# Performance work log

Measured on AMD Instinct MI355X. Metric: run time of the kernel, lower is better.

The kernel has to match this reference:

```python
import jax, jax.numpy as jnp
import numpy as np

B, F, T, Z, Y, X = 1, 8, 5, 16, 96, 96
N_RAYS = 32768   # n_rays_scan
K = 128          # n_points_ray
NEAR_PLANE = 0.01
C = F * Z        # conv channels after folding Z into channel dim


def setup_inputs() -> dict:
    key = jax.random.key(0)
    ks = jax.random.split(key, 6)
    vol = jax.random.normal(ks[0], (B, F, T, Z, Y, X), jnp.float32)
    # ray origins inside the normalized unit-cube scene
    rays_o = jax.random.uniform(ks[1], (T, N_RAYS, 3), jnp.float32, 0.1, 0.9)
    rd = jax.random.normal(ks[2], (T, N_RAYS, 3), jnp.float32)
    rays_d = rd / jnp.linalg.norm(rd, axis=-1, keepdims=True)
    conv_w = jax.random.normal(ks[3], (C, C, 3, 3, 3), jnp.float32) * (1.0 / np.sqrt(C * 27))
    conv_b = jnp.zeros((C,), jnp.float32)
    dens_w = jax.random.normal(ks[4], (F, 1), jnp.float32) * (1.0 / np.sqrt(F))
    dens_b = jnp.zeros((1,), jnp.float32)
    return dict(curr_feat_volume=vol, ray_start=rays_o, ray_direction=rays_d,
                conv_w=conv_w, conv_b=conv_b, dens_w=dens_w, dens_b=dens_b)


def _trilinear(vol, pts):
    """vol: [F,Z,Y,X]; pts: [...,3] with (x,y,z) in [0,1]. Returns [..., F]."""
    Fc, Zs, Ys, Xs = vol.shape
    gx = jnp.clip(pts[..., 0], 0.0, 1.0) * (Xs - 1)
    gy = jnp.clip(pts[..., 1], 0.0, 1.0) * (Ys - 1)
    gz = jnp.clip(pts[..., 2], 0.0, 1.0) * (Zs - 1)
    x0 = jnp.floor(gx).astype(jnp.int32); x1 = jnp.minimum(x0 + 1, Xs - 1)
    y0 = jnp.floor(gy).astype(jnp.int32); y1 = jnp.minimum(y0 + 1, Ys - 1)
    z0 = jnp.floor(gz).astype(jnp.int32); z1 = jnp.minimum(z0 + 1, Zs - 1)
    fx = gx - x0; fy = gy - y0; fz = gz - z0
    out = 0.0
    for zi, wz in ((z0, 1 - fz), (z1, fz)):
        for yi, wy in ((y0, 1 - fy), (y1, fy)):
            for xi, wx in ((x0, 1 - fx), (x1, fx)):
                out = out + vol[:, zi, yi, xi] * (wz * wy * wx)[None]
    return jnp.moveaxis(out, 0, -1)


def _render_t(vol_t, o, d, dens_w, dens_b):
    """One timestep: vol_t [F,Z,Y,X], o/d [N,3] -> depth [N,1]."""
    # SceneCollider: AABB [0,1]^3 with near_plane clamp
    t1 = (0.0 - o) / d
    t2 = (1.0 - o) / d
    near = jnp.max(jnp.minimum(t1, t2), axis=-1, keepdims=True)
    far = jnp.min(jnp.maximum(t1, t2), axis=-1, keepdims=True)
    near = jnp.maximum(near, NEAR_PLANE)
    far = jnp.maximum(far, near + 1e-6)
    # UniformSampler (deterministic bins)
    bins = jnp.linspace(0.0, 1.0, K + 1, dtype=jnp.float32)
    ts = near + bins[None, :] * (far - near)          # [N,K+1]
    starts = ts[:, :-1, None]                          # [N,K,1]
    ends = ts[:, 1:, None]
    mids = 0.5 * (starts + ends)
    pts = o[:, None, :] + d[:, None, :] * mids         # [N,K,3]
    # DensityField: trilinear feature gather + linear + softplus
    feats = _trilinear(vol_t, pts)                     # [N,K,F]
    density = jax.nn.softplus(feats @ dens_w + dens_b) # [N,K,1]
    # weights / transmittance (alpha compositing)
    deltas = ends - starts
    dd = density * deltas
    trans = jnp.exp(-jnp.concatenate([jnp.zeros_like(dd[:, :1]),
                                      jnp.cumsum(dd[:, :-1], axis=1)], axis=1))
    alpha = 1.0 - jnp.exp(-dd)
    weights = alpha * trans                            # [N,K,1]
    # DepthRenderer
    eps = 1e-10
    depth = jnp.sum(weights * starts, axis=-2) / (jnp.sum(weights, axis=-2) + eps)
    depth = jnp.clip(depth, starts.min(), starts.max())
    return depth                                       # [N,1]


def reference(curr_feat_volume, ray_start, ray_direction, conv_w, conv_b, dens_w, dens_b):
    # fold Z into channels and run dense Conv3d over (T,Y,X)
    x = jnp.transpose(curr_feat_volume, (0, 1, 3, 2, 4, 5)).reshape(B, F * Z, T, Y, X)
    y = jax.lax.conv_general_dilated(
        x, conv_w, window_strides=(1, 1, 1), padding='SAME',
        dimension_numbers=('NCDHW', 'OIDHW', 'NCDHW'))
    y = y + conv_b[None, :, None, None, None]
    future = jnp.transpose(y.reshape(B, F, Z, T, Y, X), (0, 3, 1, 2, 4, 5))  # [B,T,F,Z,Y,X]
    vols = future[0]                                   # [T,F,Z,Y,X]
    depth = jax.vmap(lambda v, o, d: _render_t(v, o, d, dens_w, dens_b))(
        vols, ray_start, ray_direction)                # [T,N,1]
    return depth
```

## Files before the change

### kernel.cpp

```cpp
#include <hip/hip_runtime.h>
#include <hip/hip_fp16.h>
#include <cstdint>
#include <cstddef>

#define T_DIM 5
#define F_DIM 8
#define Z_DIM 16
#define Y_DIM 96
#define X_DIM 96
#define NRAYS 32768
#define K_SAMP 128


struct __align__(16) Cell { __half2 h0, h1, h2, h3; };

typedef __attribute__((ext_vector_type(4))) float     f32x4;
typedef __attribute__((ext_vector_type(8))) _Float16  f16x8;

__device__ __forceinline__ float fexp2(float x) { return __builtin_amdgcn_exp2f(x); }
__device__ __forceinline__ float flog2(float x) { return __builtin_amdgcn_logf(x); }

__global__ __launch_bounds__(256) void setup_kernel(
        const float* __restrict__ xin, __half* __restrict__ inp,
        const float* __restrict__ w, const float* __restrict__ cb,
        const float* __restrict__ dw, __half* __restrict__ wB, float* __restrict__ bR,
        const float* __restrict__ ro, const float* __restrict__ rd,
        float* __restrict__ nearA, float* __restrict__ farA) {
    int b = blockIdx.x;
    if (b < 480) {
        __shared__ __half lds[96 * 136];
        int t = b / 96, y = b - (b / 96) * 96;
        for (int i = threadIdx.x; i < 12288; i += 256) {
            int row = i / 96;
            int x   = i - row * 96;
            int f = row >> 4, z = row & 15;
            float v = xin[(((size_t)(f * 5 + t) * 16 + z) * 96 + y) * 96 + x];
            lds[x * 136 + row] = __float2half(v);
        }
        __syncthreads();
        __half* ob = inp + ((size_t)(t * 96 + y) * 96) * 128;
        for (int c = threadIdx.x; c < 1536; c += 256) {
            int x = c >> 4, sub = c & 15;
            uint4 v = *(const uint4*)(lds + x * 136 + sub * 8);
            *(uint4*)(ob + (size_t)x * 128 + sub * 8) = v;
        }
    } else if (b < 696) {
        int i = (b - 480) * 256 + threadIdx.x;
        if (i < 16) {
            float s = 0.f;
            #pragma unroll
            for (int f = 0; f < 8; ++f) s += cb[f * 16 + i] * dw[f];
            bR[i] = s;
        }
        int cs  = i & 31;
        int zo  = (i >> 5) & 15;
        int pt  = i >> 9;
        int p   = pt / 27;
        int tap = pt - p * 27;
        int ci  = p * 32 + cs;
        float s = 0.f;
        #pragma unroll
        for (int f = 0; f < 8; ++f)
            s += w[(size_t)((f * 16 + zo) * 128 + ci) * 27 + tap] * dw[f];
        wB[i] = __float2half(s);
    } else {
        int gid = (b - 696) * 256 + threadIdx.x;
        const float* o = ro + (size_t)gid * 3;
        const float* d = rd + (size_t)gid * 3;
        float ox = o[0], oy = o[1], oz = o[2];
        float dx = d[0], dy = d[1], dz = d[2];
        float t1x = (0.f - ox) / dx, t2x = (1.f - ox) / dx;
        float t1y = (0.f - oy) / dy, t2y = (1.f - oy) / dy;
        float t1z = (0.f - oz) / dz, t2z = (1.f - oz) / dz;
        float nr = fmaxf(fmaxf(fminf(t1x, t2x), fminf(t1y, t2y)), fminf(t1z, t2z));
        float fr = fminf(fminf(fmaxf(t1x, t2x), fmaxf(t1y, t2y)), fmaxf(t1z, t2z));
        nr = fmaxf(nr, 0.01f);
        fr = fmaxf(fr, nr + 1e-6f);
        nearA[gid] = nr;
        farA[gid]  = fr;
    }
}

__global__ __launch_bounds__(128) void conv_mfma_kernel(
        const __half* __restrict__ inp, const __half* __restrict__ wB,
        float* __restrict__ part) {
    int bid = blockIdx.x;
    int wg  = (bid & 7) * 360 + (bid >> 3);
    int p   = wg & 3;
    int wq  = wg >> 2;
    int xs  = wq % 3;
    int rem = wq / 3;
    int yp  = rem % 48;
    int t   = rem / 48;
    int xseg = xs * 32, y0 = yp * 2;

    __shared__ __half lds[12 * 34 * 32];
    const int w    = threadIdx.x >> 6;
    const int lane = threadIdx.x & 63;
    const int l15  = lane & 15;
    const int ksub = lane >> 4;

    const int xl0 = threadIdx.x >> 2, sub0 = threadIdx.x & 3;
    const int xg0 = xseg + xl0 - 1;
    const bool xok0 = (unsigned)xg0 < 96u;
    const int glo0 = xg0 * 128 + sub0 * 8 + (p << 5);
    const int lof0 = xl0 * 32 + ((sub0 ^ ((xl0 >> 1) & 3)) << 3);
    const int q    = threadIdx.x / 12;
    const int rowh = threadIdx.x - q * 12;
    const int xl1  = 32 + (q >> 2), sub1 = q & 3;
    const int xg1  = xseg + xl1 - 1;
    const bool hwr = (q < 8);
    const bool hld = hwr && ((unsigned)xg1 < 96u);
    const int glo1 = xg1 * 128 + sub1 * 8 + (p << 5);
    const int lof1 = xl1 * 32 + ((sub1 ^ ((xl1 >> 1) & 3)) << 3);

    int offA[3];
    #pragma unroll
    for (int kx = 0; kx < 3; ++kx) {
        int X = l15 + kx;
        offA[kx] = X * 32 + ((ksub ^ ((X >> 1) & 3)) << 3);
    }

    uint4 vm[12];
    #pragma unroll
    for (int r = 0; r < 12; ++r) {
        int tt = t + (r >> 2) - 1;
        int yy = y0 + (r & 3) - 1;
        bool rok = ((unsigned)tt < 5u) & ((unsigned)yy < 96u);
        int rbase = (tt * 96 + yy) * 12288;
        uint4 v = {0u, 0u, 0u, 0u};
        if (rok & xok0) v = *(const uint4*)(inp + rbase + glo0);
        vm[r] = v;
    }
    uint4 vh = {0u, 0u, 0u, 0u};
    {
        int tt = t + (rowh >> 2) - 1;
        int yy = y0 + (rowh & 3) - 1;
        bool rok = ((unsigned)tt < 5u) & ((unsigned)yy < 96u);
        int rbase = (tt * 96 + yy) * 12288;
        if (rok & hld) vh = *(const uint4*)(inp + rbase + glo1);
    }
    #pragma unroll
    for (int r = 0; r < 12; ++r)
        *(uint4*)(lds + r * 1088 + lof0) = vm[r];
    if (hwr)
        *(uint4*)(lds + rowh * 1088 + lof1) = vh;
    __syncthreads();

    f32x4 acc0 = {0.f, 0.f, 0.f, 0.f};
    f32x4 acc1 = {0.f, 0.f, 0.f, 0.f};
    const __half* wp_base = wB + (size_t)p * 13824 + l15 * 32 + ksub * 8;
    #pragma unroll
    for (int kt = 0; kt < 3; ++kt) {
        #pragma unroll
        for (int ky = 0; ky < 3; ++ky) {
            const __half* lrow = lds + (kt * 4 + w + ky) * 1088;
            #pragma unroll
            for (int kx = 0; kx < 3; ++kx) {
                int tap = (kt * 3 + ky) * 3 + kx;
                f16x8 aw = *(const f16x8*)(wp_base + tap * 512);
                f16x8 b0 = *(const f16x8*)(lrow + offA[kx]);
                acc0 = __builtin_amdgcn_mfma_f32_16x16x32_f16(aw, b0, acc0, 0, 0, 0);
                f16x8 b1 = *(const f16x8*)(lrow + offA[kx] + 512);
                acc1 = __builtin_amdgcn_mfma_f32_16x16x32_f16(aw, b1, acc1, 0, 0, 0);
            }
        }
    }

    int yw = y0 + w;
    float* po = part + (size_t)p * 737280;
    #pragma unroll
    for (int r = 0; r < 4; ++r) {
        int zo = ksub * 4 + r;
        size_t o = (((size_t)t * 16 + zo) * 96 + yw) * 96 + xseg + l15;
        po[o]      = acc0[r];
        po[o + 16] = acc1[r];
    }
}

__global__ __launch_bounds__(256) void combpack_kernel(
        const float* __restrict__ part, const float* __restrict__ bR,
        Cell* __restrict__ cellp) {
    int b = blockIdx.x;
    int t = b / 192;
    int r = b - t * 192;
    int z = r / 12;
    int y0 = (r - z * 12) * 8;
    int z1 = min(z + 1, 15);

    __shared__ float Lf[18 * 96];
    const float4* pp = (const float4*)part;
    for (int j = threadIdx.x; j < 432; j += 256) {
        int row = j / 24, xq = j - row * 24;
        int plane = row >= 9;
        int zz = plane ? z1 : z;
        int yy = min(y0 + row - (plane ? 9 : 0), 95);
        size_t f4 = ((size_t)(t * 16 + zz) * 96 + yy) * 24 + xq;
        float bz = bR[zz];
        float4 a0 = pp[f4];
        float4 a1 = pp[f4 + 184320];
        float4 a2 = pp[f4 + 2 * 184320];
        float4 a3 = pp[f4 + 3 * 184320];
        float4 s;
        s.x = bz + a0.x + a1.x + a2.x + a3.x;
        s.y = bz + a0.y + a1.y + a2.y + a3.y;
        s.z = bz + a0.z + a1.z + a2.z + a3.z;
        s.w = bz + a0.w + a1.w + a2.w + a3.w;
        *(float4*)(Lf + row * 96 + xq * 4) = s;
    }
    __syncthreads();

    const size_t tz = (size_t)(t * 16 + z);
    #pragma unroll
    for (int k = 0; k < 3; ++k) {
        int c = threadIdx.x + k * 256;
        int yl = c / 96, x = c - yl * 96;
        int xp = min(x + 1, 95);
        float c000 = Lf[yl * 96 + x],        c001 = Lf[yl * 96 + xp];
        float c010 = Lf[(yl + 1) * 96 + x],  c011 = Lf[(yl + 1) * 96 + xp];
        float c100 = Lf[(9 + yl) * 96 + x],  c101 = Lf[(9 + yl) * 96 + xp];
        float c110 = Lf[(10 + yl) * 96 + x], c111 = Lf[(10 + yl) * 96 + xp];
        Cell cl;
        cl.h0 = __floats2half2_rn(c000, c001 - c000);
        cl.h1 = __floats2half2_rn(c010, c011 - c010);
        cl.h2 = __floats2half2_rn(c100, c101 - c100);
        cl.h3 = __floats2half2_rn(c110, c111 - c110);
        cellp[(tz * 96 + y0 + yl) * 96 + x] = cl;
    }
}

__global__ __launch_bounds__(256) void render_kernel(
        const float* __restrict__ ro, const float* __restrict__ rd,
        const Cell* __restrict__ cellp,
        const float* __restrict__ nearA, const float* __restrict__ farA,
        const float* __restrict__ dens_b, float* __restrict__ out) {
    int b = blockIdx.x;
    int b7 = b & 7, bhi = b >> 3;
    int t, seg;
    if (b7 < 5) { t = b7; seg = bhi; }
    else { int j = (b7 - 5) * 640 + bhi; t = j / 384; seg = 640 + j % 384; }
    int c = threadIdx.x & 7;
    int ray = t * NRAYS + seg * 32 + (threadIdx.x >> 3);

    const float* o = ro + (size_t)ray * 3;
    const float* d = rd + (size_t)ray * 3;
    float ox = o[0], oy = o[1], oz = o[2];
    float dx = d[0], dy = d[1], dz = d[2];
    float nr = nearA[ray], fr = farA[ray];
    const Cell* vt = cellp + (size_t)t * 147456;
    const float L2E = 1.4426950408889634f;
    float db2 = dens_b[0] * L2E;

    float span = fr - nr;
    float step = span * 0.0078125f;
    float s  = fmaf((float)(c * 16), step, nr);
    float mid = s + 0.5f * step;
    float pxg = fmaf(dx, mid, ox) * 95.f;
    float pyg = fmaf(dy, mid, oy) * 95.f;
    float pzg = fmaf(dz, mid, oz) * 15.f;
    float ddxg = dx * step * 95.f, ddyg = dy * step * 95.f, ddzg = dz * step * 15.f;

    float num = 0.f, den = 0.f, A2 = 0.f;
    float trans = 1.f;
    int pidx = -1;
    Cell cl;
    for (int kk = 0; kk < 16; ++kk) {
        int x0 = min(max((int)pxg, 0), 94);
        int y0 = min(max((int)pyg, 0), 94);
        int z0 = min(max((int)pzg, 0), 14);
        float fx = pxg - (float)x0, fy = pyg - (float)y0, fz = pzg - (float)z0;

        int idx = z0 * 9216 + y0 * 96 + x0;
        if (idx != pidx) {
            pidx = idx;
            cl = vt[idx];
        }

        float v00 = fmaf(fx, __half2float(__high2half(cl.h0)), __half2float(__low2half(cl.h0)));
        float v01 = fmaf(fx, __half2float(__high2half(cl.h1)), __half2float(__low2half(cl.h1)));
        float v10 = fmaf(fx, __half2float(__high2half(cl.h2)), __half2float(__low2half(cl.h2)));
        float v11 = fmaf(fx, __half2float(__high2half(cl.h3)), __half2float(__low2half(cl.h3)));
        float v0  = fmaf(fy, v01 - v00, v00);
        float v1  = fmaf(fy, v11 - v10, v10);
        float pre2 = fmaf(fmaf(fz, v1 - v0, v0), L2E, db2);

        float u = fexp2(-fabsf(pre2));
        float dens2 = fmaxf(pre2, 0.f) + flog2(1.f + u);
        float dd2 = dens2 * step;
        float ex = fexp2(-dd2);
        float wgt = (1.f - ex) * trans;
        num = fmaf(wgt, s, num);
        den += wgt;
        trans *= ex;
        A2 += dd2;
        s += step; pxg += ddxg; pyg += ddyg; pzg += ddzg;
    }
    int lane = threadIdx.x & 63;
    int qb = lane & ~7;
    float P = 0.f;
    #pragma unroll
    for (int j = 0; j < 7; ++j) {
        float Aj = __shfl(A2, qb + j, 64);
        P += (c > j) ? Aj : 0.f;
    }
    float sc = fexp2(-P);
    float numc = num * sc;
    float denc = den * sc;
    numc += __shfl_xor(numc, 1, 64);
    numc += __shfl_xor(numc, 2, 64);
    numc += __shfl_xor(numc, 4, 64);
    denc += __shfl_xor(denc, 1, 64);
    denc += __shfl_xor(denc, 2, 64);
    denc += __shfl_xor(denc, 4, 64);
    if (c == 0) {
        float depth = numc / (denc + 1e-10f);
        float slast = fmaf(0.9921875f, span, nr);
        depth = fminf(fmaxf(depth, nr), slast);
        out[ray] = depth;
    }
}

extern "C" void kernel_launch(void* const* d_in, const int* in_sizes, int n_in,
                              void* d_out, int out_size, void* d_ws, size_t ws_size,
                              hipStream_t stream) {
    const float* vol = (const float*)d_in[0];
    const float* ro  = (const float*)d_in[1];
    const float* rd  = (const float*)d_in[2];
    const float* cw  = (const float*)d_in[3];
    const float* cb  = (const float*)d_in[4];
    const float* dw  = (const float*)d_in[5];
    const float* dbp = (const float*)d_in[6];
    float* out = (float*)d_out;

    float* ws      = (float*)d_ws;
    __half* inp    = (__half*)(ws + 737280);
    Cell*  cellp   = (Cell*)(ws + 737280);
    __half* wB     = (__half*)(ws + 737280 + 2949120);
    float* bR      = ws + 737280 + 2949120 + 27648;
    float* nearA   = bR + 32;
    float* farA    = nearA + 163840;
    float* part    = farA + 163840;

    hipLaunchKernelGGL(setup_kernel, dim3(1336), dim3(256), 0, stream,
                       vol, inp, cw, cb, dw, wB, bR, ro, rd, nearA, farA);
    hipLaunchKernelGGL(conv_mfma_kernel, dim3(2880), dim3(128), 0, stream,
                       inp, wB, part);
    hipLaunchKernelGGL(combpack_kernel, dim3(960), dim3(256), 0, stream,
                       part, bR, cellp);
    hipLaunchKernelGGL(render_kernel, dim3(5120), dim3(256), 0, stream,
                       ro, rd, cellp, nearA, farA, dbp, out);
}
```

Measured before the change: 157.0 us.

## Enlarge conv tile to four output rows and rewrite input transpose without LDS

```diff
diff --git a/kernel.cpp b/kernel.cpp
--- a/kernel.cpp
+++ b/kernel.cpp
@@ -27,25 +27,25 @@
         const float* __restrict__ ro, const float* __restrict__ rd,
         float* __restrict__ nearA, float* __restrict__ farA) {
     int b = blockIdx.x;
-    if (b < 480) {
-        __shared__ __half lds[96 * 136];
-        int t = b / 96, y = b - (b / 96) * 96;
-        for (int i = threadIdx.x; i < 12288; i += 256) {
-            int row = i / 96;
-            int x   = i - row * 96;
-            int f = row >> 4, z = row & 15;
-            float v = xin[(((size_t)(f * 5 + t) * 16 + z) * 96 + y) * 96 + x];
-            lds[x * 136 + row] = __float2half(v);
+    if (b < 1440) {
+        int idx = b * 256 + threadIdx.x;
+        int f = idx / 46080;
+        int r = idx - f * 46080;
+        int t = r / 9216;
+        int yx = r - t * 9216;
+        const float* src = xin + (size_t)f * 737280 + t * 147456 + yx;
+        __half2 h[8];
+        #pragma unroll
+        for (int zp = 0; zp < 8; ++zp) {
+            float v0 = src[(size_t)(2 * zp) * 9216];
+            float v1 = src[(size_t)(2 * zp + 1) * 9216];
+            h[zp] = __floats2half2_rn(v0, v1);
         }
-        __syncthreads();
-        __half* ob = inp + ((size_t)(t * 96 + y) * 96) * 128;
-        for (int c = threadIdx.x; c < 1536; c += 256) {
-            int x = c >> 4, sub = c & 15;
-            uint4 v = *(const uint4*)(lds + x * 136 + sub * 8);
-            *(uint4*)(ob + (size_t)x * 128 + sub * 8) = v;
-        }
-    } else if (b < 696) {
-        int i = (b - 480) * 256 + threadIdx.x;
+        __half* dst = inp + (size_t)r * 128 + f * 16;
+        *(uint4*)(dst)     = *(uint4*)&h[0];
+        *(uint4*)(dst + 8) = *(uint4*)&h[4];
+    } else if (b < 1656) {
+        int i = (b - 1440) * 256 + threadIdx.x;
         if (i < 16) {
             float s = 0.f;
             #pragma unroll
@@ -64,7 +64,7 @@
             s += w[(size_t)((f * 16 + zo) * 128 + ci) * 27 + tap] * dw[f];
         wB[i] = __float2half(s);
     } else {
-        int gid = (b - 696) * 256 + threadIdx.x;
+        int gid = (b - 1656) * 256 + threadIdx.x;
         const float* o = ro + (size_t)gid * 3;
         const float* d = rd + (size_t)gid * 3;
         float ox = o[0], oy = o[1], oz = o[2];
@@ -81,35 +81,38 @@
     }
 }
 
-__global__ __launch_bounds__(128) void conv_mfma_kernel(
+__global__ __launch_bounds__(256) void conv_mfma_kernel(
         const __half* __restrict__ inp, const __half* __restrict__ wB,
         float* __restrict__ part) {
     int bid = blockIdx.x;
-    int wg  = (bid & 7) * 360 + (bid >> 3);
+    int wg  = (bid & 7) * 180 + (bid >> 3);
     int p   = wg & 3;
     int wq  = wg >> 2;
     int xs  = wq % 3;
     int rem = wq / 3;
-    int yp  = rem % 48;
-    int t   = rem / 48;
-    int xseg = xs * 32, y0 = yp * 2;
-
-    __shared__ __half lds[12 * 34 * 32];
-    const int w    = threadIdx.x >> 6;
-    const int lane = threadIdx.x & 63;
+    int yq  = rem % 24;
+    int t   = rem / 24;
+    int xseg = xs * 32, y0 = yq * 4;
+
+    __shared__ __half lds[18 * 34 * 32];
+    const int tid  = threadIdx.x;
+    const int w    = tid >> 6;
+    const int lane = tid & 63;
     const int l15  = lane & 15;
     const int ksub = lane >> 4;
 
-    const int xl0 = threadIdx.x >> 2, sub0 = threadIdx.x & 3;
+    const int col = tid & 127;
+    const int xl0 = col >> 2, sub0 = col & 3;
+    const int rg  = tid >> 7;
     const int xg0 = xseg + xl0 - 1;
     const bool xok0 = (unsigned)xg0 < 96u;
     const int glo0 = xg0 * 128 + sub0 * 8 + (p << 5);
     const int lof0 = xl0 * 32 + ((sub0 ^ ((xl0 >> 1) & 3)) << 3);
-    const int q    = threadIdx.x / 12;
-    const int rowh = threadIdx.x - q * 12;
+    const int q    = tid / 18;
+    const int rowh = tid - q * 18;
+    const bool hwr = (tid < 144);
     const int xl1  = 32 + (q >> 2), sub1 = q & 3;
     const int xg1  = xseg + xl1 - 1;
-    const bool hwr = (q < 8);
     const bool hld = hwr && ((unsigned)xg1 < 96u);
     const int glo1 = xg1 * 128 + sub1 * 8 + (p << 5);
     const int lof1 = xl1 * 32 + ((sub1 ^ ((xl1 >> 1) & 3)) << 3);
@@ -121,28 +124,29 @@
         offA[kx] = X * 32 + ((ksub ^ ((X >> 1) & 3)) << 3);
     }
 
-    uint4 vm[12];
-    #pragma unroll
-    for (int r = 0; r < 12; ++r) {
-        int tt = t + (r >> 2) - 1;
-        int yy = y0 + (r & 3) - 1;
+    uint4 vm[9];
+    #pragma unroll
+    for (int rr = 0; rr < 9; ++rr) {
+        int r = rg * 9 + rr;
+        int tt = t + r / 6 - 1;
+        int yy = y0 + r % 6 - 1;
         bool rok = ((unsigned)tt < 5u) & ((unsigned)yy < 96u);
         int rbase = (tt * 96 + yy) * 12288;
         uint4 v = {0u, 0u, 0u, 0u};
         if (rok & xok0) v = *(const uint4*)(inp + rbase + glo0);
-        vm[r] = v;
+        vm[rr] = v;
     }
     uint4 vh = {0u, 0u, 0u, 0u};
     {
-        int tt = t + (rowh >> 2) - 1;
-        int yy = y0 + (rowh & 3) - 1;
+        int tt = t + rowh / 6 - 1;
+        int yy = y0 + rowh % 6 - 1;
         bool rok = ((unsigned)tt < 5u) & ((unsigned)yy < 96u);
         int rbase = (tt * 96 + yy) * 12288;
         if (rok & hld) vh = *(const uint4*)(inp + rbase + glo1);
     }
     #pragma unroll
-    for (int r = 0; r < 12; ++r)
-        *(uint4*)(lds + r * 1088 + lof0) = vm[r];
+    for (int rr = 0; rr < 9; ++rr)
+        *(uint4*)(lds + (rg * 9 + rr) * 1088 + lof0) = vm[rr];
     if (hwr)
         *(uint4*)(lds + rowh * 1088 + lof1) = vh;
     __syncthreads();
@@ -154,7 +158,7 @@
     for (int kt = 0; kt < 3; ++kt) {
         #pragma unroll
         for (int ky = 0; ky < 3; ++ky) {
-            const __half* lrow = lds + (kt * 4 + w + ky) * 1088;
+            const __half* lrow = lds + (kt * 6 + w + ky) * 1088;
             #pragma unroll
             for (int kx = 0; kx < 3; ++kx) {
                 int tap = (kt * 3 + ky) * 3 + kx;
@@ -341,9 +345,9 @@
     float* farA    = nearA + 163840;
     float* part    = farA + 163840;
 
-    hipLaunchKernelGGL(setup_kernel, dim3(1336), dim3(256), 0, stream,
+    hipLaunchKernelGGL(setup_kernel, dim3(2296), dim3(256), 0, stream,
                        vol, inp, cw, cb, dw, wB, bR, ro, rd, nearA, farA);
-    hipLaunchKernelGGL(conv_mfma_kernel, dim3(2880), dim3(128), 0, stream,
+    hipLaunchKernelGGL(conv_mfma_kernel, dim3(1440), dim3(256), 0, stream,
                        inp, wB, part);
     hipLaunchKernelGGL(combpack_kernel, dim3(960), dim3(256), 0, stream,
                        part, bR, cellp);
```

Result: no change. 157.4 us (median of 2 runs) (+0.2%).
